# Kernel tuning notes

Measured on AMD Instinct MI355X. Metric: run time of the kernel, lower is better.

The kernel has to match this reference:

```python
import jax, jax.numpy as jnp
import numpy as np

D = 768
CTX = 64


def ln(x, g, b, eps=1e-5):
    m = x.mean(-1, keepdims=True)
    v = jnp.mean((x - m) ** 2, -1, keepdims=True)
    return (x - m) / jnp.sqrt(v + eps) * g + b


def setup_inputs() -> dict:
    key = jax.random.key(0)
    ks = jax.random.split(key, 16)
    B, N = 16, 1024
    w = lambda k, shape: jax.random.normal(k, shape, dtype=jnp.float32) * 0.02
    return {
        'comps': jax.random.normal(ks[0], (8, B, N, D), jnp.float32),
        'geometric_context': jax.random.normal(ks[1], (B, N, D), jnp.float32),
        'question_features': jax.random.normal(ks[2], (B, D), jnp.float32),
        'spatial_mask': jax.random.randint(ks[3], (B,), 0, 2) > 0,
        'gp_w1': w(ks[4], (D, D // 2)), 'gp_b1': jnp.zeros((D // 2,)),
        'gp_g1': jnp.ones((D // 2,)), 'gp_be1': jnp.zeros((D // 2,)),
        'gp_w2': w(ks[5], (D // 2, CTX)), 'gp_b2': jnp.zeros((CTX,)),
        'swp_w1': w(ks[6], (CTX + D, 256)), 'swp_b1': jnp.zeros((256,)),
        'swp_g1': jnp.ones((256,)), 'swp_be1': jnp.zeros((256,)),
        'swp_w2': w(ks[7], (256, 128)), 'swp_b2': jnp.zeros((128,)),
        'swp_g2': jnp.ones((128,)), 'swp_be2': jnp.zeros((128,)),
        'swp_w3': w(ks[8], (128, 8)), 'swp_b3': jnp.zeros((8,)),
        'sw1': w(ks[9], (4, D + CTX, D)), 'sb1': jnp.zeros((4, D)),
        'sg1': jnp.ones((4, D)), 'sbe1': jnp.zeros((4, D)),
        'sw2': w(ks[10], (4, D, D)), 'sb2': jnp.zeros((4, D)),
        'sg2': jnp.ones((4, D)), 'sbe2': jnp.zeros((4, D)),
        'rw1': w(ks[11], (4, D + CTX, D)), 'rb1': jnp.zeros((4, D)),
        'rg1': jnp.ones((4, D)), 'rbe1': jnp.zeros((4, D)),
        'rw2': w(ks[12], (4, D, D)), 'rb2': jnp.zeros((4, D)),
    }


def reference(comps, geometric_context, question_features, spatial_mask,
              gp_w1, gp_b1, gp_g1, gp_be1, gp_w2, gp_b2,
              swp_w1, swp_b1, swp_g1, swp_be1, swp_w2, swp_b2, swp_g2, swp_be2, swp_w3, swp_b3,
              sw1, sb1, sg1, sbe1, sw2, sb2, sg2, sbe2,
              rw1, rb1, rg1, rbe1, rw2, rb2):
    B, N = geometric_context.shape[:2]
    # geometric_processor on mean-pooled context -> [B, 64]
    gcc = jax.nn.relu(ln(geometric_context.mean(1) @ gp_w1 + gp_b1, gp_g1, gp_be1)) @ gp_w2 + gp_b2
    # spatial_weight_predictor -> softmax weights [B, 8]
    wi = jnp.concatenate([gcc, question_features], -1)
    h = jax.nn.gelu(ln(wi @ swp_w1 + swp_b1, swp_g1, swp_be1), approximate=False)
    h = jax.nn.gelu(ln(h @ swp_w2 + swp_b2, swp_g2, swp_be2), approximate=False)
    aw = jax.nn.softmax(h @ swp_w3 + swp_b3, -1)
    # expanded context; non-spatial samples use 0.1-scaled context for spatial-set comps
    ctx = jnp.broadcast_to(gcc[:, None, :], (B, N, CTX))
    ctx_s = ctx * jnp.where(spatial_mask, 1.0, 0.1)[:, None, None]
    # strong enhancers (GELU, second LN): P_unique(0), V_unique(1), PV(3), PT(5) - all spatial-set
    xs = jnp.concatenate([comps[jnp.array([0, 1, 3, 5])],
                          jnp.broadcast_to(ctx_s, (4, B, N, CTX))], -1)
    h = jax.nn.gelu(ln(jnp.einsum('kbnd,kdf->kbnf', xs, sw1) + sb1[:, None, None, :],
                       sg1[:, None, None, :], sbe1[:, None, None, :]), approximate=False)
    ys = ln(jnp.einsum('kbnd,kdf->kbnf', h, sw2) + sb2[:, None, None, :],
            sg2[:, None, None, :], sbe2[:, None, None, :])
    # ReLU enhancers (moderate/minimal share structure): TV(4, scaled ctx), T_unique(2), redundant(6), higher(7)
    ctx_r = jnp.stack([ctx_s, ctx, ctx, ctx], 0)
    xr = jnp.concatenate([comps[jnp.array([4, 2, 6, 7])], ctx_r], -1)
    h = jax.nn.relu(ln(jnp.einsum('kbnd,kdf->kbnf', xr, rw1) + rb1[:, None, None, :],
                       rg1[:, None, None, :], rbe1[:, None, None, :]))
    yr = jnp.einsum('kbnd,kdf->kbnf', h, rw2) + rb2[:, None, None, :]
    # non-spatial components pass through when spatial_mask is False
    m = spatial_mask[:, None, None]
    out = jnp.stack([
        ys[0],                              # P_unique
        ys[1],                              # V_unique
        jnp.where(m, yr[1], comps[2]),      # T_unique
        ys[2],                              # PV_synergy
        yr[0],                              # TV_synergy
        ys[3],                              # PT_synergy
        jnp.where(m, yr[2], comps[6]),      # redundant
        jnp.where(m, yr[3], comps[7]),      # higher_synergy
    ], 0)
    return out, aw
```

## Files before the change

kernel.cpp:

```cpp
#include <hip/hip_runtime.h>
#include <math.h>

#define MT 16384
#define DD 768
#define AW_OFF ((size_t)8 * MT * DD)

typedef __attribute__((ext_vector_type(8))) short short8;
typedef __attribute__((ext_vector_type(4))) float f32x4;
typedef __attribute__((ext_vector_type(4))) float fv4;
typedef __attribute__((ext_vector_type(4))) unsigned int u32x4;

#define OFF_W1T 0ULL
#define OFF_W2T 10223616ULL
#define OFF_Z1  19660800ULL
#define OFF_Z2  220987392ULL
#define OFF_GB  321650688ULL
#define OFF_P1  321675264ULL
#define OFF_P2  324820992ULL
#define OFF_ST1 326393856ULL
#define OFF_ST2 327442432ULL
#define OFF_GP  327966720ULL
#define OFF_GM  328359936ULL
#define OFF_CXS 328409088ULL
#define OFF_CXU 328411136ULL

static __device__ __forceinline__ unsigned short f2bf(float f) {
  unsigned u = __float_as_uint(f);
  u += 0x7fffu + ((u >> 16) & 1u);
  return (unsigned short)(u >> 16);
}
static __device__ __forceinline__ float bf2f(unsigned short h) {
  return __uint_as_float(((unsigned)h) << 16);
}
static __device__ __forceinline__ unsigned pk2(float lo, float hi) {
  return (unsigned)f2bf(lo) | ((unsigned)f2bf(hi) << 16);
}
static __device__ __forceinline__ float gelu_t(float y) {
  float y2 = y * y;
  float c = fmaf(y2, 0.0713548163f, 1.59576912161f);
  float e = __expf(-y * c);
  return y / (1.0f + e);
}
static __device__ __forceinline__ void gload_lds16(const void* g, void* l) {
  __builtin_amdgcn_global_load_lds(
      (const __attribute__((address_space(1))) void*)g,
      (__attribute__((address_space(3))) void*)l, 16, 0, 0);
}

__global__ void transpose_cvt(const float* sw1, const float* rw1,
                              const float* sw2, const float* rw2,
                              unsigned short* w1T, unsigned short* w2T) {
  __shared__ float t[32][33];
  const int z = blockIdx.z;
  int R; const float* sp; unsigned short* dp;
  if (z < 8) {
    R = 832;
    sp = ((z < 4) ? sw1 : rw1) + (size_t)(z & 3) * 832 * DD;
    dp = w1T + (size_t)z * DD * 832;
  } else {
    R = 768;
    int zz = z - 8;
    sp = ((zz < 4) ? sw2 : rw2) + (size_t)(zz & 3) * DD * DD;
    dp = w2T + (size_t)zz * DD * DD;
  }
  const int r0 = blockIdx.x * 32, c0 = blockIdx.y * 32;
  if (r0 >= R) return;
  const int tx = threadIdx.x & 31, ty = threadIdx.x >> 5;
#pragma unroll
  for (int i = 0; i < 4; i++) {
    int r = ty + i * 8;
    t[r][tx] = sp[(size_t)(r0 + r) * DD + c0 + tx];
  }
  __syncthreads();
#pragma unroll
  for (int i = 0; i < 4; i++) {
    int cc = ty + i * 8;
    dp[(size_t)(c0 + cc) * R + r0 + tx] = f2bf(t[tx][cc]);
  }
}

__global__ void pack_gb(const float* sg1, const float* sbe1,
                        const float* rg1, const float* rbe1,
                        unsigned short* gb1) {
  const int k = blockIdx.x * 256 + threadIdx.x;
  const int br = blockIdx.y;
  const float* gs = ((br < 4) ? sg1 : rg1) + (br & 3) * DD;
  const float* bs = ((br < 4) ? sbe1 : rbe1) + (br & 3) * DD;
  gb1[((size_t)br * DD + k) * 2]     = f2bf(gs[k]);
  gb1[((size_t)br * DD + k) * 2 + 1] = f2bf(bs[k]);
}

__global__ void colmean1(const float* __restrict__ geo, float* __restrict__ gp) {
  const int b = blockIdx.z, yc = blockIdx.y;
  const int col = blockIdx.x * 256 + threadIdx.x;
  const float* p = geo + (size_t)b * 1024 * DD + (size_t)yc * 128 * DD + col;
  float s = 0.f;
  for (int n = 0; n < 128; ++n) s += p[(size_t)n * DD];
  gp[((size_t)b * 8 + yc) * DD + col] = s;
}
__global__ void colmean2(const float* __restrict__ gp, float* __restrict__ gm) {
  const int b = blockIdx.y;
  const int col = blockIdx.x * 256 + threadIdx.x;
  float s = 0.f;
#pragma unroll
  for (int i = 0; i < 8; ++i) s += gp[((size_t)b * 8 + i) * DD + col];
  gm[(size_t)b * DD + col] = s * (1.0f / 1024.0f);
}

static __device__ float2 blk_sum2(float a, float b, float* red) {
  const int tid = threadIdx.x;
  __syncthreads();
  red[tid] = a; red[512 + tid] = b;
  if (tid < 128) { red[384 + tid] = 0.f; red[512 + 384 + tid] = 0.f; }
  __syncthreads();
  for (int s = 256; s > 0; s >>= 1) {
    if (tid < s) { red[tid] += red[tid + s]; red[512 + tid] += red[512 + tid + s]; }
    __syncthreads();
  }
  return make_float2(red[0], red[512]);
}

__global__ void small_mlp(
    const float* __restrict__ gc_mean, const float* __restrict__ qf,
    const int* __restrict__ mask,
    const float* __restrict__ gp_w1, const float* __restrict__ gp_b1,
    const float* __restrict__ gp_g1, const float* __restrict__ gp_be1,
    const float* __restrict__ gp_w2, const float* __restrict__ gp_b2,
    const float* __restrict__ swp_w1, const float* __restrict__ swp_b1,
    const float* __restrict__ swp_g1, const float* __restrict__ swp_be1,
    const float* __restrict__ swp_w2, const float* __restrict__ swp_b2,
    const float* __restrict__ swp_g2, const float* __restrict__ swp_be2,
    const float* __restrict__ swp_w3, const float* __restrict__ swp_b3,
    unsigned short* __restrict__ ctxs, unsigned short* __restrict__ ctxu,
    float* __restrict__ aw)
{
  __shared__ float gm[768];
  __shared__ float buf[832];
  __shared__ float tmp[384];
  __shared__ float red[1024];
  const int b = blockIdx.x, tid = threadIdx.x;

  for (int i = tid; i < 768; i += 384) gm[i] = gc_mean[b * 768 + i];
  __syncthreads();

  float z = gp_b1[tid];
  for (int k = 0; k < 768; k++) z += gm[k] * gp_w1[k * 384 + tid];
  float2 s = blk_sum2(z, z * z, red);
  {
    float mean = s.x * (1.f / 384.f);
    float rinv = rsqrtf(s.y * (1.f / 384.f) - mean * mean + 1e-5f);
    float y = (z - mean) * rinv * gp_g1[tid] + gp_be1[tid];
    tmp[tid] = fmaxf(y, 0.f);
  }
  __syncthreads();

  if (tid < 64) {
    float g = gp_b2[tid];
    for (int k = 0; k < 384; k++) g += tmp[k] * gp_w2[k * 64 + tid];
    float sc = (mask[b] != 0) ? 1.0f : 0.1f;
    ctxs[b * 64 + tid] = f2bf(g * sc);
    ctxu[b * 64 + tid] = f2bf(g);
    buf[tid] = g;
  }
  for (int i = tid; i < 768; i += 384) buf[64 + i] = qf[b * 768 + i];
  __syncthreads();

  float z1 = 0.f;
  if (tid < 256) {
    z1 = swp_b1[tid];
    for (int k = 0; k < 832; k++) z1 += buf[k] * swp_w1[k * 256 + tid];
  }
  s = blk_sum2(z1, z1 * z1, red);
  {
    float mean = s.x * (1.f / 256.f);
    float rinv = rsqrtf(s.y * (1.f / 256.f) - mean * mean + 1e-5f);
    if (tid < 256) {
      float y = (z1 - mean) * rinv * swp_g1[tid] + swp_be1[tid];
      tmp[tid] = 0.5f * y * (1.f + erff(y * 0.7071067811865476f));
    }
  }
  __syncthreads();

  float z2 = 0.f;
  if (tid < 128) {
    z2 = swp_b2[tid];
    for (int k = 0; k < 256; k++) z2 += tmp[k] * swp_w2[k * 128 + tid];
  }
  s = blk_sum2(z2, z2 * z2, red);
  {
    float mean = s.x * (1.f / 128.f);
    float rinv = rsqrtf(s.y * (1.f / 128.f) - mean * mean + 1e-5f);
    if (tid < 128) {
      float y = (z2 - mean) * rinv * swp_g2[tid] + swp_be2[tid];
      tmp[tid] = 0.5f * y * (1.f + erff(y * 0.7071067811865476f));
    }
  }
  __syncthreads();

  if (tid < 8) {
    float z3 = swp_b3[tid];
    for (int k = 0; k < 128; k++) z3 += tmp[k] * swp_w3[k * 8 + tid];
    buf[tid] = z3;
  }
  __syncthreads();
  if (tid < 8) {
    float mx = buf[0];
    for (int k = 1; k < 8; k++) mx = fmaxf(mx, buf[k]);
    float ssum = 0.f;
    for (int k = 0; k < 8; k++) ssum += expf(buf[k] - mx);
    aw[b * 8 + tid] = expf(buf[tid] - mx) / ssum;
  }
}

__global__ void stats_k(const float2* __restrict__ part, float2* __restrict__ st,
                        int nr) {
  int i = blockIdx.x * 256 + threadIdx.x;
  if (i >= nr) return;
  float2 p0 = part[i], p1 = part[nr + i], p2 = part[2 * nr + i];
  float s1 = p0.x + p1.x + p2.x, s2 = p0.y + p1.y + p2.y;
  float mean = s1 * (1.f / 768.f);
  float var = s2 * (1.f / 768.f) - mean * mean;
  float rinv = rsqrtf(var + 1e-5f);
  st[i] = make_float2(rinv, -mean * rinv);
}

__global__ __launch_bounds__(512, 2)
void gemm1_k(const float* __restrict__ comps,
             const unsigned short* __restrict__ cxs,
             const unsigned short* __restrict__ cxu,
             const unsigned short* __restrict__ w1T,
             const float* __restrict__ sb1, const float* __restrict__ rb1,
             unsigned short* __restrict__ z1,
             float2* __restrict__ part1,
             const int* __restrict__ mask)
{
  __shared__ __align__(16) unsigned short As[3][8192];
  __shared__ __align__(16) unsigned short Bs[3][8192];
  __shared__ float pscr[4][256][2];
  constexpr int NT = 26;

  const int id = blockIdx.x;
  const int x = id & 7, j = id >> 3;
  const int br_nt = j >> 3;
  const int mt = ((j & 7) << 3) | x;
  const int nt = br_nt % 3;
  const int br = br_nt / 3;
  const int m0 = mt * 256, n0 = nt * 256;
  const int b = m0 >> 10;
  const int msk = mask[b];
  if (br >= 5 && msk == 0) return;

  const int ci = (0x76245310u >> (br * 4)) & 15;
  const float* afp = comps + (size_t)ci * MT * DD + (size_t)m0 * DD;
  const unsigned short* ctxp = ((br <= 4) ? cxs : cxu) + b * 64;
  const unsigned short* wT = w1T + (size_t)br * DD * 832 + (size_t)n0 * 832;
  const float* bias = ((br < 4) ? sb1 : rb1) + (br & 3) * DD;
  unsigned short* zo = z1 + (size_t)br * MT * DD + (size_t)m0 * DD;

  const int tid = threadIdx.x;
  const int w = tid >> 6, lane = tid & 63, llo = lane & 15, lhi = lane >> 4;
  const int wm = w & 1, wn = w >> 1;
  const int q = tid & 3, rr = tid >> 2;
  const int swq = q ^ ((tid >> 3) & 3);

  const unsigned short* bsrc0 = wT + (size_t)rr * 832 + swq * 8;
  const unsigned short* bsrc1 = wT + (size_t)(128 + rr) * 832 + swq * 8;
  const float* asrc0 = afp + (size_t)rr * DD + q * 8;
  const float* asrc1 = afp + (size_t)(128 + rr) * DD + q * 8;
  const unsigned short* csrc = ctxp + q * 8;

  f32x4 acc[8][4];
#pragma unroll
  for (int mf = 0; mf < 8; ++mf)
#pragma unroll
    for (int nf = 0; nf < 4; ++nf) acc[mf][nf] = (f32x4)0.0f;

  struct St { fv4 f0, f1, f2, f3; u32x4 c; };

  auto issueB = [&](int kt, int s) {
    gload_lds16(bsrc0 + (size_t)kt * 32, &Bs[s][w * 512]);
    gload_lds16(bsrc1 + (size_t)kt * 32, &Bs[s][4096 + w * 512]);
  };
  auto issueA = [&](int kt) -> St {
    St s;
    if (kt < 24) {
      const float* p0 = asrc0 + kt * 32;
      s.f0 = *(const fv4*)p0; s.f1 = *(const fv4*)(p0 + 4);
      const float* p1 = asrc1 + kt * 32;
      s.f2 = *(const fv4*)p1; s.f3 = *(const fv4*)(p1 + 4);
    } else {
      s.c = *(const u32x4*)(csrc + (kt - 24) * 32);
    }
    return s;
  };
  auto commitA = [&](const St& s, int kt, int sl) {
    u32x4* d0 = (u32x4*)&As[sl][rr * 32 + swq * 8];
    u32x4* d1 = (u32x4*)&As[sl][(128 + rr) * 32 + swq * 8];
    if (kt < 24) {
      u32x4 v0, v1;
      v0[0] = pk2(s.f0[0], s.f0[1]); v0[1] = pk2(s.f0[2], s.f0[3]);
      v0[2] = pk2(s.f1[0], s.f1[1]); v0[3] = pk2(s.f1[2], s.f1[3]);
      v1[0] = pk2(s.f2[0], s.f2[1]); v1[1] = pk2(s.f2[2], s.f2[3]);
      v1[2] = pk2(s.f3[0], s.f3[1]); v1[3] = pk2(s.f3[2], s.f3[3]);
      *d0 = v0; *d1 = v1;
    } else {
      *d0 = s.c; *d1 = s.c;
    }
  };
  const int aswz = (lhi ^ ((llo >> 1) & 3)) << 3;
  const int arow0 = (wm * 128 + llo) * 32 + aswz;
  const int brow0 = (wn * 64 + llo) * 32 + aswz;
  auto compute = [&](int sl) {
    const unsigned short* Ab = &As[sl][0];
    const unsigned short* Bb = &Bs[sl][0];
    short8 bfr[4];
#pragma unroll
    for (int nf = 0; nf < 4; ++nf) bfr[nf] = *(const short8*)&Bb[brow0 + nf * 512];
#pragma unroll
    for (int mf = 0; mf < 8; ++mf) {
      short8 a = *(const short8*)&Ab[arow0 + mf * 512];
#pragma unroll
      for (int nf = 0; nf < 4; ++nf)
        acc[mf][nf] = __builtin_amdgcn_mfma_f32_16x16x32_bf16(a, bfr[nf], acc[mf][nf], 0, 0, 0);
    }
  };

  issueB(0, 0);
  __builtin_amdgcn_sched_barrier(0);
  St s0 = issueA(0);
  __builtin_amdgcn_sched_barrier(0);
  issueB(1, 1);
  __builtin_amdgcn_sched_barrier(0);
  St s1 = issueA(1);
  __builtin_amdgcn_sched_barrier(0);
  commitA(s0, 0, 0);
  asm volatile("s_waitcnt lgkmcnt(0)" ::: "memory");
  __builtin_amdgcn_sched_barrier(0);
  __builtin_amdgcn_s_barrier();

  St sCur = s1;
  int sl = 0;
#pragma unroll 1
  for (int t = 0; t < NT; ++t) {
    int sl1 = sl + 1; if (sl1 == 3) sl1 = 0;
    int sl2 = sl1 + 1; if (sl2 == 3) sl2 = 0;
    St sNxt = sCur;
    if (t + 2 < NT) {
      issueB(t + 2, sl2);
      __builtin_amdgcn_sched_barrier(0);
      sNxt = issueA(t + 2);
      __builtin_amdgcn_sched_barrier(0);
    }
    if (t + 1 < NT) commitA(sCur, t + 1, sl1);
    compute(sl);
    asm volatile("s_waitcnt lgkmcnt(0)" ::: "memory");
    __builtin_amdgcn_sched_barrier(0);
    __builtin_amdgcn_s_barrier();
    sCur = sNxt; sl = sl1;
  }

  const int n0w = n0 + wn * 64;
  float bia[4];
#pragma unroll
  for (int nf = 0; nf < 4; ++nf) bia[nf] = bias[n0w + nf * 16 + llo];
#pragma unroll
  for (int mf = 0; mf < 8; ++mf) {
#pragma unroll
    for (int r = 0; r < 4; ++r) {
      float zz[4]; float s1v = 0.f, s2v = 0.f;
#pragma unroll
      for (int nf = 0; nf < 4; ++nf) {
        float zv = acc[mf][nf][r] + bia[nf];
        zz[nf] = zv; s1v += zv; s2v += zv * zv;
      }
      const int rloc = wm * 128 + mf * 16 + lhi * 4 + r;
      const size_t rowoff = (size_t)rloc * DD;
#pragma unroll
      for (int nf = 0; nf < 4; ++nf) {
        float zon = __shfl_xor(zz[nf], 1);
        if ((llo & 1) == 0)
          *(unsigned*)&zo[rowoff + n0w + nf * 16 + llo] = pk2(zz[nf], zon);
      }
#pragma unroll
      for (int d = 1; d < 16; d <<= 1) {
        s1v += __shfl_xor(s1v, d); s2v += __shfl_xor(s2v, d);
      }
      if (llo == 0) { pscr[wn][rloc][0] = s1v; pscr[wn][rloc][1] = s2v; }
    }
  }
  __syncthreads();
  if (tid < 256) {
    float a = 0.f, c = 0.f;
#pragma unroll
    for (int qq = 0; qq < 4; ++qq) { a += pscr[qq][tid][0]; c += pscr[qq][tid][1]; }
    part1[(size_t)nt * (8 * MT) + (size_t)br * MT + m0 + tid] = make_float2(a, c);
  }
}

template<int SBR>
__global__ __launch_bounds__(512, 2)
void gemm2_k(const float* __restrict__ comps,
             const unsigned short* __restrict__ z1,
             const float2* __restrict__ st1,
             const unsigned short* __restrict__ gb1,
             const unsigned short* __restrict__ w2T,
             const float* __restrict__ sb2, const float* __restrict__ rb2,
             unsigned short* __restrict__ z2,
             float2* __restrict__ part2,
             float* __restrict__ outp,
             const int* __restrict__ mask)
{
  __shared__ __align__(16) unsigned short As[3][8192];
  __shared__ __align__(16) unsigned short Bs[3][8192];
  __shared__ float pscr[4][256][2];
  constexpr int NT = 24;

  const int id = blockIdx.x;
  const int x = id & 7, j = id >> 3;
  const int br_nt = j >> 3;
  const int mt = ((j & 7) << 3) | x;
  const int nt = br_nt % 3;
  const int brl = br_nt / 3;
  const int br = SBR ? brl : (brl + 4);
  const int m0 = mt * 256, n0 = nt * 256;
  const int b = m0 >> 10;
  const int msk = mask[b];
  const int ci = (0x76245310u >> (br * 4)) & 15;
  const int tid = threadIdx.x;

  if (!SBR && br >= 5 && msk == 0) {
    const float* cs = comps + (size_t)ci * MT * DD + (size_t)m0 * DD + n0;
    float* cd = outp + (size_t)ci * MT * DD + (size_t)m0 * DD + n0;
#pragma unroll 1
    for (int k = 0; k < 32; ++k) {
      int idx = tid + k * 512;
      int r2 = idx >> 6, c4 = (idx & 63) * 4;
      *(fv4*)(cd + (size_t)r2 * DD + c4) = *(const fv4*)(cs + (size_t)r2 * DD + c4);
    }
    return;
  }

  const unsigned short* az = z1 + (size_t)br * MT * DD + (size_t)m0 * DD;
  const unsigned short* wT = w2T + (size_t)br * DD * DD + (size_t)n0 * DD;
  const float* bias = (SBR ? sb2 : rb2) + (br & 3) * DD;

  const int w = tid >> 6, lane = tid & 63, llo = lane & 15, lhi = lane >> 4;
  const int wm = w & 1, wn = w >> 1;
  const int q = tid & 3, rr = tid >> 2;
  const int swq = q ^ ((tid >> 3) & 3);

  const unsigned short* bsrc0 = wT + (size_t)rr * DD + swq * 8;
  const unsigned short* bsrc1 = wT + (size_t)(128 + rr) * DD + swq * 8;
  const unsigned short* zsrc0 = az + (size_t)rr * DD + q * 8;
  const unsigned short* zsrc1 = az + (size_t)(128 + rr) * DD + q * 8;
  const unsigned short* gsrc = gb1 + (size_t)br * DD * 2 + q * 16;
  const float2 stv0 = st1[(size_t)br * MT + m0 + rr];
  const float2 stv1 = st1[(size_t)br * MT + m0 + 128 + rr];

  f32x4 acc[8][4];
#pragma unroll
  for (int mf = 0; mf < 8; ++mf)
#pragma unroll
    for (int nf = 0; nf < 4; ++nf) acc[mf][nf] = (f32x4)0.0f;

  struct St { u32x4 z0, z1v, g0, g1; };

  auto issueB = [&](int kt, int s) {
    gload_lds16(bsrc0 + (size_t)kt * 32, &Bs[s][w * 512]);
    gload_lds16(bsrc1 + (size_t)kt * 32, &Bs[s][4096 + w * 512]);
  };
  auto issueA = [&](int kt) -> St {
    St s;
    s.z0  = *(const u32x4*)(zsrc0 + kt * 32);
    s.z1v = *(const u32x4*)(zsrc1 + kt * 32);
    s.g0  = *(const u32x4*)(gsrc + kt * 64);
    s.g1  = *(const u32x4*)(gsrc + kt * 64 + 8);
    return s;
  };
  auto xform2 = [&](unsigned zw, unsigned gwa, unsigned gwb, float2 stv) -> unsigned {
    float z0 = bf2f((unsigned short)(zw & 0xffffu));
    float z1f = bf2f((unsigned short)(zw >> 16));
    float g0 = bf2f((unsigned short)(gwa & 0xffffu));
    float be0 = bf2f((unsigned short)(gwa >> 16));
    float g1 = bf2f((unsigned short)(gwb & 0xffffu));
    float be1 = bf2f((unsigned short)(gwb >> 16));
    float y0 = fmaf(fmaf(z0, stv.x, stv.y), g0, be0);
    float y1 = fmaf(fmaf(z1f, stv.x, stv.y), g1, be1);
    if (SBR) { y0 = gelu_t(y0); y1 = gelu_t(y1); }
    else     { y0 = fmaxf(y0, 0.f); y1 = fmaxf(y1, 0.f); }
    return pk2(y0, y1);
  };
  auto commitA2 = [&](const St& s, int sl) {
    u32x4 v0, v1;
    v0[0] = xform2(s.z0[0], s.g0[0], s.g0[1], stv0);
    v0[1] = xform2(s.z0[1], s.g0[2], s.g0[3], stv0);
    v0[2] = xform2(s.z0[2], s.g1[0], s.g1[1], stv0);
    v0[3] = xform2(s.z0[3], s.g1[2], s.g1[3], stv0);
    v1[0] = xform2(s.z1v[0], s.g0[0], s.g0[1], stv1);
    v1[1] = xform2(s.z1v[1], s.g0[2], s.g0[3], stv1);
    v1[2] = xform2(s.z1v[2], s.g1[0], s.g1[1], stv1);
    v1[3] = xform2(s.z1v[3], s.g1[2], s.g1[3], stv1);
    *(u32x4*)&As[sl][rr * 32 + swq * 8] = v0;
    *(u32x4*)&As[sl][(128 + rr) * 32 + swq * 8] = v1;
  };

  const int aswz = (lhi ^ ((llo >> 1) & 3)) << 3;
  const int arow0 = (wm * 128 + llo) * 32 + aswz;
  const int brow0 = (wn * 64 + llo) * 32 + aswz;
  auto compute = [&](int sl) {
    const unsigned short* Ab = &As[sl][0];
    const unsigned short* Bb = &Bs[sl][0];
    short8 bfr[4];
#pragma unroll
    for (int nf = 0; nf < 4; ++nf) bfr[nf] = *(const short8*)&Bb[brow0 + nf * 512];
#pragma unroll
    for (int mf = 0; mf < 8; ++mf) {
      short8 a = *(const short8*)&Ab[arow0 + mf * 512];
#pragma unroll
      for (int nf = 0; nf < 4; ++nf)
        acc[mf][nf] = __builtin_amdgcn_mfma_f32_16x16x32_bf16(a, bfr[nf], acc[mf][nf], 0, 0, 0);
    }
  };

  issueB(0, 0);
  __builtin_amdgcn_sched_barrier(0);
  St s0 = issueA(0);
  __builtin_amdgcn_sched_barrier(0);
  issueB(1, 1);
  __builtin_amdgcn_sched_barrier(0);
  St s1 = issueA(1);
  __builtin_amdgcn_sched_barrier(0);
  commitA2(s0, 0);
  asm volatile("s_waitcnt lgkmcnt(0)" ::: "memory");
  __builtin_amdgcn_sched_barrier(0);
  __builtin_amdgcn_s_barrier();

  St sCur = s1;
  int sl = 0;
#pragma unroll 1
  for (int t = 0; t < NT; ++t) {
    int sl1 = sl + 1; if (sl1 == 3) sl1 = 0;
    int sl2 = sl1 + 1; if (sl2 == 3) sl2 = 0;
    St sNxt = sCur;
    if (t + 2 < NT) {
      issueB(t + 2, sl2);
      __builtin_amdgcn_sched_barrier(0);
      sNxt = issueA(t + 2);
      __builtin_amdgcn_sched_barrier(0);
    }
    if (t + 1 < NT) commitA2(sCur, sl1);
    compute(sl);
    asm volatile("s_waitcnt lgkmcnt(0)" ::: "memory");
    __builtin_amdgcn_sched_barrier(0);
    __builtin_amdgcn_s_barrier();
    sCur = sNxt; sl = sl1;
  }

  const int n0w = n0 + wn * 64;
  float bia[4];
#pragma unroll
  for (int nf = 0; nf < 4; ++nf) bia[nf] = bias[n0w + nf * 16 + llo];

  if (SBR) {
    unsigned short* zo = z2 + (size_t)br * MT * DD + (size_t)m0 * DD;
#pragma unroll
    for (int mf = 0; mf < 8; ++mf) {
#pragma unroll
      for (int r = 0; r < 4; ++r) {
        float zz[4]; float s1v = 0.f, s2v = 0.f;
#pragma unroll
        for (int nf = 0; nf < 4; ++nf) {
          float zv = acc[mf][nf][r] + bia[nf];
          zz[nf] = zv; s1v += zv; s2v += zv * zv;
        }
        const int rloc = wm * 128 + mf * 16 + lhi * 4 + r;
        const size_t rowoff = (size_t)rloc * DD;
#pragma unroll
        for (int nf = 0; nf < 4; ++nf) {
          float zon = __shfl_xor(zz[nf], 1);
          if ((llo & 1) == 0)
            *(unsigned*)&zo[rowoff + n0w + nf * 16 + llo] = pk2(zz[nf], zon);
        }
#pragma unroll
        for (int d = 1; d < 16; d <<= 1) {
          s1v += __shfl_xor(s1v, d); s2v += __shfl_xor(s2v, d);
        }
        if (llo == 0) { pscr[wn][rloc][0] = s1v; pscr[wn][rloc][1] = s2v; }
      }
    }
    __syncthreads();
    if (tid < 256) {
      float a = 0.f, c = 0.f;
#pragma unroll
      for (int qq = 0; qq < 4; ++qq) { a += pscr[qq][tid][0]; c += pscr[qq][tid][1]; }
      part2[(size_t)nt * (4 * MT) + (size_t)br * MT + m0 + tid] = make_float2(a, c);
    }
  } else {
    float* fo = outp + (size_t)ci * MT * DD + (size_t)m0 * DD;
#pragma unroll
    for (int mf = 0; mf < 8; ++mf) {
#pragma unroll
      for (int r = 0; r < 4; ++r) {
        const int rloc = wm * 128 + mf * 16 + lhi * 4 + r;
        const size_t rowoff = (size_t)rloc * DD;
#pragma unroll
        for (int nf = 0; nf < 4; ++nf)
          fo[rowoff + n0w + nf * 16 + llo] = acc[mf][nf][r] + bia[nf];
      }
    }
  }
}

__global__ void finish_s(const unsigned short* __restrict__ z2,
                         const float2* __restrict__ st2,
                         const float* __restrict__ sg2,
                         const float* __restrict__ sbe2,
                         float* __restrict__ outp)
{
  const int tid = threadIdx.x;
  const int rowg = blockIdx.x * 8 + (tid >> 5);
  const int l = tid & 31;
  const int br = rowg >> 14;
  const int r = rowg & 16383;
  const int ci = (0x5310u >> (br * 4)) & 15;
  const unsigned short* zp = z2 + (size_t)rowg * DD;
  float* op = outp + (size_t)ci * MT * DD + (size_t)r * DD;
  const float2 stv = st2[rowg];
  const float* g = sg2 + br * DD;
  const float* be = sbe2 + br * DD;
#pragma unroll
  for (int c = 0; c < 3; ++c) {
    const int col = l * 8 + c * 256;
    u32x4 zv = *(const u32x4*)(zp + col);
    fv4 ga = *(const fv4*)(g + col), gb = *(const fv4*)(g + col + 4);
    fv4 ba = *(const fv4*)(be + col), bb = *(const fv4*)(be + col + 4);
    fv4 o0, o1;
#pragma unroll
    for (int wd = 0; wd < 2; ++wd) {
      o0[2 * wd]     = fmaf(fmaf(bf2f((unsigned short)(zv[wd] & 0xffffu)), stv.x, stv.y), ga[2 * wd], ba[2 * wd]);
      o0[2 * wd + 1] = fmaf(fmaf(bf2f((unsigned short)(zv[wd] >> 16)), stv.x, stv.y), ga[2 * wd + 1], ba[2 * wd + 1]);
      o1[2 * wd]     = fmaf(fmaf(bf2f((unsigned short)(zv[wd + 2] & 0xffffu)), stv.x, stv.y), gb[2 * wd], bb[2 * wd]);
      o1[2 * wd + 1] = fmaf(fmaf(bf2f((unsigned short)(zv[wd + 2] >> 16)), stv.x, stv.y), gb[2 * wd + 1], bb[2 * wd + 1]);
    }
    *(fv4*)(op + col) = o0;
    *(fv4*)(op + col + 4) = o1;
  }
}

extern "C" void kernel_launch(void* const* d_in, const int* in_sizes, int n_in,
                              void* d_out, int out_size, void* d_ws, size_t ws_size,
                              hipStream_t stream)
{
  (void)in_sizes; (void)n_in; (void)out_size; (void)ws_size;
  const float* comps  = (const float*)d_in[0];
  const float* geo    = (const float*)d_in[1];
  const float* qf     = (const float*)d_in[2];
  const int*   mask   = (const int*)d_in[3];
  const float* gp_w1  = (const float*)d_in[4];
  const float* gp_b1  = (const float*)d_in[5];
  const float* gp_g1  = (const float*)d_in[6];
  const float* gp_be1 = (const float*)d_in[7];
  const float* gp_w2  = (const float*)d_in[8];
  const float* gp_b2  = (const float*)d_in[9];
  const float* swp_w1 = (const float*)d_in[10];
  const float* swp_b1 = (const float*)d_in[11];
  const float* swp_g1 = (const float*)d_in[12];
  const float* swp_be1= (const float*)d_in[13];
  const float* swp_w2 = (const float*)d_in[14];
  const float* swp_b2 = (const float*)d_in[15];
  const float* swp_g2 = (const float*)d_in[16];
  const float* swp_be2= (const float*)d_in[17];
  const float* swp_w3 = (const float*)d_in[18];
  const float* swp_b3 = (const float*)d_in[19];
  const float* sw1 = (const float*)d_in[20];
  const float* sb1 = (const float*)d_in[21];
  const float* sg1 = (const float*)d_in[22];
  const float* sbe1= (const float*)d_in[23];
  const float* sw2 = (const float*)d_in[24];
  const float* sb2 = (const float*)d_in[25];
  const float* sg2 = (const float*)d_in[26];
  const float* sbe2= (const float*)d_in[27];
  const float* rw1 = (const float*)d_in[28];
  const float* rb1 = (const float*)d_in[29];
  const float* rg1 = (const float*)d_in[30];
  const float* rbe1= (const float*)d_in[31];
  const float* rw2 = (const float*)d_in[32];
  const float* rb2 = (const float*)d_in[33];
  float* out = (float*)d_out;

  char* ws = (char*)d_ws;
  unsigned short* w1T = (unsigned short*)(ws + OFF_W1T);
  unsigned short* w2T = (unsigned short*)(ws + OFF_W2T);
  unsigned short* z1  = (unsigned short*)(ws + OFF_Z1);
  unsigned short* z2  = (unsigned short*)(ws + OFF_Z2);
  unsigned short* gb1 = (unsigned short*)(ws + OFF_GB);
  float2* part1 = (float2*)(ws + OFF_P1);
  float2* part2 = (float2*)(ws + OFF_P2);
  float2* st1   = (float2*)(ws + OFF_ST1);
  float2* st2   = (float2*)(ws + OFF_ST2);
  float* gpart  = (float*)(ws + OFF_GP);
  float* gmean  = (float*)(ws + OFF_GM);
  unsigned short* cxs = (unsigned short*)(ws + OFF_CXS);
  unsigned short* cxu = (unsigned short*)(ws + OFF_CXU);

  transpose_cvt<<<dim3(26, 24, 16), 256, 0, stream>>>(sw1, rw1, sw2, rw2, w1T, w2T);
  pack_gb<<<dim3(3, 8), 256, 0, stream>>>(sg1, sbe1, rg1, rbe1, gb1);
  colmean1<<<dim3(3, 8, 16), 256, 0, stream>>>(geo, gpart);
  colmean2<<<dim3(3, 16), 256, 0, stream>>>(gpart, gmean);
  small_mlp<<<16, 384, 0, stream>>>(gmean, qf, mask,
      gp_w1, gp_b1, gp_g1, gp_be1, gp_w2, gp_b2,
      swp_w1, swp_b1, swp_g1, swp_be1, swp_w2, swp_b2, swp_g2, swp_be2,
      swp_w3, swp_b3, cxs, cxu, out + AW_OFF);

  hipMemsetAsync(part1, 0, 3 * 8 * MT * sizeof(float2), stream);
  hipMemsetAsync(part2, 0, 3 * 4 * MT * sizeof(float2), stream);

  gemm1_k<<<1536, 512, 0, stream>>>(comps, cxs, cxu, w1T, sb1, rb1, z1, part1, mask);
  stats_k<<<512, 256, 0, stream>>>(part1, st1, 8 * MT);
  gemm2_k<1><<<768, 512, 0, stream>>>(comps, z1, st1, gb1, w2T, sb2, rb2,
                                      z2, part2, out, mask);
  gemm2_k<0><<<768, 512, 0, stream>>>(comps, z1, st1, gb1, w2T, sb2, rb2,
                                      z2, part2, out, mask);
  stats_k<<<256, 256, 0, stream>>>(part2, st2, 4 * MT);
  finish_s<<<8192, 256, 0, stream>>>(z2, st2, sg2, sbe2, out);
}
```

Baseline: 950.6 us.

## Split LN1+activation into separate kernel, shrink GEMM M-tile, direct-to-LDS A loads

Moves the first LayerNorm normalization and GELU/ReLU out of the second GEMM's A-load path into a standalone act1_k kernel that writes a bf16 activation buffer. With that buffer, gemm2 can stream A straight into LDS like B does, using a 3-stage pipeline. Both GEMMs switch to 128-row M tiles with a 4-block occupancy hint, gemm1 drops to double buffering, and the two templated gemm2 launches merge into one. The cost is an extra full read and write of the z1-sized activation tensor plus an extra launch. The part1/part2 memsets are removed, which relies on every partial-sum slot being overwritten each call.

After: 774.7 us. 1.23x faster.

```diff
diff --git a/kernel.cpp b/kernel.cpp
--- a/kernel.cpp
+++ b/kernel.cpp
@@ -14,7 +14,6 @@
 #define OFF_W2T 10223616ULL
 #define OFF_Z1  19660800ULL
 #define OFF_Z2  220987392ULL
-#define OFF_GB  321650688ULL
 #define OFF_P1  321675264ULL
 #define OFF_P2  324820992ULL
 #define OFF_ST1 326393856ULL
@@ -23,6 +22,7 @@
 #define OFF_GM  328359936ULL
 #define OFF_CXS 328409088ULL
 #define OFF_CXU 328411136ULL
+#define OFF_A1  335544320ULL
 
 static __device__ __forceinline__ unsigned short f2bf(float f) {
   unsigned u = __float_as_uint(f);
@@ -77,17 +77,6 @@
     int cc = ty + i * 8;
     dp[(size_t)(c0 + cc) * R + r0 + tx] = f2bf(t[tx][cc]);
   }
-}
-
-__global__ void pack_gb(const float* sg1, const float* sbe1,
-                        const float* rg1, const float* rbe1,
-                        unsigned short* gb1) {
-  const int k = blockIdx.x * 256 + threadIdx.x;
-  const int br = blockIdx.y;
-  const float* gs = ((br < 4) ? sg1 : rg1) + (br & 3) * DD;
-  const float* bs = ((br < 4) ? sbe1 : rbe1) + (br & 3) * DD;
-  gb1[((size_t)br * DD + k) * 2]     = f2bf(gs[k]);
-  gb1[((size_t)br * DD + k) * 2 + 1] = f2bf(bs[k]);
 }
 
 __global__ void colmean1(const float* __restrict__ geo, float* __restrict__ gp) {
@@ -224,7 +213,7 @@
   st[i] = make_float2(rinv, -mean * rinv);
 }
 
-__global__ __launch_bounds__(512, 2)
+__global__ __launch_bounds__(512, 4)
 void gemm1_k(const float* __restrict__ comps,
              const unsigned short* __restrict__ cxs,
              const unsigned short* __restrict__ cxu,
@@ -234,137 +223,128 @@
              float2* __restrict__ part1,
              const int* __restrict__ mask)
 {
-  __shared__ __align__(16) unsigned short As[3][8192];
-  __shared__ __align__(16) unsigned short Bs[3][8192];
-  __shared__ float pscr[4][256][2];
+  __shared__ __align__(16) unsigned short As[2][4096];
+  __shared__ __align__(16) unsigned short Bs[2][8192];
+  __shared__ float pscr[4][128][2];
   constexpr int NT = 26;
 
   const int id = blockIdx.x;
   const int x = id & 7, j = id >> 3;
-  const int br_nt = j >> 3;
-  const int mt = ((j & 7) << 3) | x;
+  const int br_nt = j >> 4;
+  const int mt = ((j & 15) << 3) | x;
   const int nt = br_nt % 3;
   const int br = br_nt / 3;
-  const int m0 = mt * 256, n0 = nt * 256;
+  const int m0 = mt * 128, n0 = nt * 256;
   const int b = m0 >> 10;
-  const int msk = mask[b];
-  if (br >= 5 && msk == 0) return;
+  if (br >= 5 && mask[b] == 0) return;
 
   const int ci = (0x76245310u >> (br * 4)) & 15;
   const float* afp = comps + (size_t)ci * MT * DD + (size_t)m0 * DD;
   const unsigned short* ctxp = ((br <= 4) ? cxs : cxu) + b * 64;
   const unsigned short* wT = w1T + (size_t)br * DD * 832 + (size_t)n0 * 832;
-  const float* bias = ((br < 4) ? sb1 : rb1) + (br & 3) * DD;
-  unsigned short* zo = z1 + (size_t)br * MT * DD + (size_t)m0 * DD;
 
   const int tid = threadIdx.x;
   const int w = tid >> 6, lane = tid & 63, llo = lane & 15, lhi = lane >> 4;
   const int wm = w & 1, wn = w >> 1;
-  const int q = tid & 3, rr = tid >> 2;
-  const int swq = q ^ ((tid >> 3) & 3);
-
-  const unsigned short* bsrc0 = wT + (size_t)rr * 832 + swq * 8;
-  const unsigned short* bsrc1 = wT + (size_t)(128 + rr) * 832 + swq * 8;
-  const float* asrc0 = afp + (size_t)rr * DD + q * 8;
-  const float* asrc1 = afp + (size_t)(128 + rr) * DD + q * 8;
-  const unsigned short* csrc = ctxp + q * 8;
-
-  f32x4 acc[8][4];
-#pragma unroll
-  for (int mf = 0; mf < 8; ++mf)
+
+  const int arow = tid >> 2, ap = tid & 3;
+  const int aslot = (arow * 32 + ((ap ^ ((arow >> 1) & 3)) << 3));
+  const float* asrc = afp + (size_t)arow * DD + ap * 8;
+  const unsigned short* csrc = ctxp + ap * 8;
+
+  const int q = lane & 3, rrB = w * 16 + (lane >> 2);
+  const int swqB = q ^ ((rrB >> 1) & 3);
+  const unsigned short* bsrc0 = wT + (size_t)rrB * 832 + swqB * 8;
+  const unsigned short* bsrc1 = wT + (size_t)(128 + rrB) * 832 + swqB * 8;
+
+  f32x4 acc[4][4];
+#pragma unroll
+  for (int mf = 0; mf < 4; ++mf)
 #pragma unroll
     for (int nf = 0; nf < 4; ++nf) acc[mf][nf] = (f32x4)0.0f;
 
-  struct St { fv4 f0, f1, f2, f3; u32x4 c; };
+  struct St { u32x4 q0, q1; };
 
   auto issueB = [&](int kt, int s) {
     gload_lds16(bsrc0 + (size_t)kt * 32, &Bs[s][w * 512]);
     gload_lds16(bsrc1 + (size_t)kt * 32, &Bs[s][4096 + w * 512]);
   };
-  auto issueA = [&](int kt) -> St {
+  auto loadA = [&](int kt) -> St {
     St s;
     if (kt < 24) {
-      const float* p0 = asrc0 + kt * 32;
-      s.f0 = *(const fv4*)p0; s.f1 = *(const fv4*)(p0 + 4);
-      const float* p1 = asrc1 + kt * 32;
-      s.f2 = *(const fv4*)p1; s.f3 = *(const fv4*)(p1 + 4);
+      const u32x4* p = (const u32x4*)(asrc + kt * 32);
+      s.q0 = p[0]; s.q1 = p[1];
     } else {
-      s.c = *(const u32x4*)(csrc + (kt - 24) * 32);
+      s.q0 = *(const u32x4*)(csrc + (kt - 24) * 32);
+      s.q1 = s.q0;
     }
     return s;
   };
   auto commitA = [&](const St& s, int kt, int sl) {
-    u32x4* d0 = (u32x4*)&As[sl][rr * 32 + swq * 8];
-    u32x4* d1 = (u32x4*)&As[sl][(128 + rr) * 32 + swq * 8];
+    u32x4 v;
     if (kt < 24) {
-      u32x4 v0, v1;
-      v0[0] = pk2(s.f0[0], s.f0[1]); v0[1] = pk2(s.f0[2], s.f0[3]);
-      v0[2] = pk2(s.f1[0], s.f1[1]); v0[3] = pk2(s.f1[2], s.f1[3]);
-      v1[0] = pk2(s.f2[0], s.f2[1]); v1[1] = pk2(s.f2[2], s.f2[3]);
-      v1[2] = pk2(s.f3[0], s.f3[1]); v1[3] = pk2(s.f3[2], s.f3[3]);
-      *d0 = v0; *d1 = v1;
+      v[0] = pk2(__uint_as_float(s.q0[0]), __uint_as_float(s.q0[1]));
+      v[1] = pk2(__uint_as_float(s.q0[2]), __uint_as_float(s.q0[3]));
+      v[2] = pk2(__uint_as_float(s.q1[0]), __uint_as_float(s.q1[1]));
+      v[3] = pk2(__uint_as_float(s.q1[2]), __uint_as_float(s.q1[3]));
     } else {
-      *d0 = s.c; *d1 = s.c;
-    }
+      v = s.q0;
+    }
+    *(u32x4*)&As[sl][aslot] = v;
   };
+
   const int aswz = (lhi ^ ((llo >> 1) & 3)) << 3;
-  const int arow0 = (wm * 128 + llo) * 32 + aswz;
+  const int arow0 = (wm * 64 + llo) * 32 + aswz;
   const int brow0 = (wn * 64 + llo) * 32 + aswz;
   auto compute = [&](int sl) {
-    const unsigned short* Ab = &As[sl][0];
-    const unsigned short* Bb = &Bs[sl][0];
-    short8 bfr[4];
-#pragma unroll
-    for (int nf = 0; nf < 4; ++nf) bfr[nf] = *(const short8*)&Bb[brow0 + nf * 512];
-#pragma unroll
-    for (int mf = 0; mf < 8; ++mf) {
-      short8 a = *(const short8*)&Ab[arow0 + mf * 512];
-#pragma unroll
-      for (int nf = 0; nf < 4; ++nf)
-        acc[mf][nf] = __builtin_amdgcn_mfma_f32_16x16x32_bf16(a, bfr[nf], acc[mf][nf], 0, 0, 0);
+    short8 afr[4];
+#pragma unroll
+    for (int mf = 0; mf < 4; ++mf)
+      afr[mf] = *(const short8*)&As[sl][arow0 + mf * 512];
+#pragma unroll
+    for (int nf = 0; nf < 4; ++nf) {
+      short8 bfr = *(const short8*)&Bs[sl][brow0 + nf * 512];
+#pragma unroll
+      for (int mf = 0; mf < 4; ++mf)
+        acc[mf][nf] = __builtin_amdgcn_mfma_f32_16x16x32_bf16(afr[mf], bfr, acc[mf][nf], 0, 0, 0);
     }
   };
 
   issueB(0, 0);
-  __builtin_amdgcn_sched_barrier(0);
-  St s0 = issueA(0);
-  __builtin_amdgcn_sched_barrier(0);
-  issueB(1, 1);
-  __builtin_amdgcn_sched_barrier(0);
-  St s1 = issueA(1);
-  __builtin_amdgcn_sched_barrier(0);
-  commitA(s0, 0, 0);
+  {
+    St s0 = loadA(0);
+    commitA(s0, 0, 0);
+  }
   asm volatile("s_waitcnt lgkmcnt(0)" ::: "memory");
   __builtin_amdgcn_sched_barrier(0);
   __builtin_amdgcn_s_barrier();
 
-  St sCur = s1;
-  int sl = 0;
 #pragma unroll 1
   for (int t = 0; t < NT; ++t) {
-    int sl1 = sl + 1; if (sl1 == 3) sl1 = 0;
-    int sl2 = sl1 + 1; if (sl2 == 3) sl2 = 0;
-    St sNxt = sCur;
-    if (t + 2 < NT) {
-      issueB(t + 2, sl2);
-      __builtin_amdgcn_sched_barrier(0);
-      sNxt = issueA(t + 2);
-      __builtin_amdgcn_sched_barrier(0);
-    }
-    if (t + 1 < NT) commitA(sCur, t + 1, sl1);
-    compute(sl);
+    const int cur = t & 1, nxt = cur ^ 1;
+    const bool more = (t + 1 < NT);
+    St sn;
+    if (more) {
+      issueB(t + 1, nxt);
+      sn = loadA(t + 1);
+    }
+    __builtin_amdgcn_sched_barrier(0);
+    compute(cur);
+    __builtin_amdgcn_sched_barrier(0);
+    if (more) commitA(sn, t + 1, nxt);
     asm volatile("s_waitcnt lgkmcnt(0)" ::: "memory");
     __builtin_amdgcn_sched_barrier(0);
     __builtin_amdgcn_s_barrier();
-    sCur = sNxt; sl = sl1;
-  }
-
+  }
+
+  const float* bias = ((br < 4) ? sb1 : rb1) + (br & 3) * DD;
+  unsigned short* zo = z1 + (size_t)br * MT * DD + (size_t)m0 * DD;
   const int n0w = n0 + wn * 64;
   float bia[4];
 #pragma unroll
   for (int nf = 0; nf < 4; ++nf) bia[nf] = bias[n0w + nf * 16 + llo];
 #pragma unroll
-  for (int mf = 0; mf < 8; ++mf) {
+  for (int mf = 0; mf < 4; ++mf) {
 #pragma unroll
     for (int r = 0; r < 4; ++r) {
       float zz[4]; float s1v = 0.f, s2v = 0.f;
@@ -373,7 +353,7 @@
         float zv = acc[mf][nf][r] + bia[nf];
         zz[nf] = zv; s1v += zv; s2v += zv * zv;
       }
-      const int rloc = wm * 128 + mf * 16 + lhi * 4 + r;
+      const int rloc = wm * 64 + mf * 16 + lhi * 4 + r;
       const size_t rowoff = (size_t)rloc * DD;
 #pragma unroll
       for (int nf = 0; nf < 4; ++nf) {
@@ -389,7 +369,7 @@
     }
   }
   __syncthreads();
-  if (tid < 256) {
+  if (tid < 128) {
     float a = 0.f, c = 0.f;
 #pragma unroll
     for (int qq = 0; qq < 4; ++qq) { a += pscr[qq][tid][0]; c += pscr[qq][tid][1]; }
@@ -397,12 +377,55 @@
   }
 }
 
-template<int SBR>
-__global__ __launch_bounds__(512, 2)
+__global__ void act1_k(const unsigned short* __restrict__ z1,
+                       const float2* __restrict__ st1,
+                       const float* __restrict__ sg1, const float* __restrict__ sbe1,
+                       const float* __restrict__ rg1, const float* __restrict__ rbe1,
+                       const int* __restrict__ mask,
+                       unsigned short* __restrict__ a1)
+{
+  const int tid = threadIdx.x;
+  const int rowg = blockIdx.x * 8 + (tid >> 5);
+  const int l = tid & 31;
+  const int br = rowg >> 14;
+  const int r = rowg & 16383;
+  const int b = r >> 10;
+  if (br >= 5 && mask[b] == 0) return;
+  const bool isg = (br < 4);
+  const float* g  = (isg ? sg1  + br * DD : rg1  + (br - 4) * DD);
+  const float* be = (isg ? sbe1 + br * DD : rbe1 + (br - 4) * DD);
+  const float2 stv = st1[rowg];
+  const unsigned short* zp = z1 + (size_t)rowg * DD;
+  unsigned short* op = a1 + (size_t)rowg * DD;
+#pragma unroll
+  for (int c = 0; c < 3; ++c) {
+    const int col = l * 8 + c * 256;
+    u32x4 zv = *(const u32x4*)(zp + col);
+    fv4 ga = *(const fv4*)(g + col), gb = *(const fv4*)(g + col + 4);
+    fv4 ba = *(const fv4*)(be + col), bb = *(const fv4*)(be + col + 4);
+    float y[8];
+#pragma unroll
+    for (int wd = 0; wd < 2; ++wd) {
+      y[2*wd]   = fmaf(fmaf(bf2f((unsigned short)(zv[wd] & 0xffffu)), stv.x, stv.y), ga[2*wd], ba[2*wd]);
+      y[2*wd+1] = fmaf(fmaf(bf2f((unsigned short)(zv[wd] >> 16)), stv.x, stv.y), ga[2*wd+1], ba[2*wd+1]);
+      y[4+2*wd]   = fmaf(fmaf(bf2f((unsigned short)(zv[wd+2] & 0xffffu)), stv.x, stv.y), gb[2*wd], bb[2*wd]);
+      y[4+2*wd+1] = fmaf(fmaf(bf2f((unsigned short)(zv[wd+2] >> 16)), stv.x, stv.y), gb[2*wd+1], bb[2*wd+1]);
+    }
+    u32x4 ov;
+#pragma unroll
+    for (int wd = 0; wd < 4; ++wd) {
+      float y0 = y[2*wd], y1 = y[2*wd+1];
+      if (isg) { y0 = gelu_t(y0); y1 = gelu_t(y1); }
+      else     { y0 = fmaxf(y0, 0.f); y1 = fmaxf(y1, 0.f); }
+      ov[wd] = pk2(y0, y1);
+    }
+    *(u32x4*)(op + col) = ov;
+  }
+}
+
+__global__ __launch_bounds__(512, 4)
 void gemm2_k(const float* __restrict__ comps,
-             const unsigned short* __restrict__ z1,
-             const float2* __restrict__ st1,
-             const unsigned short* __restrict__ gb1,
+             const unsigned short* __restrict__ a1,
              const unsigned short* __restrict__ w2T,
              const float* __restrict__ sb2, const float* __restrict__ rb2,
              unsigned short* __restrict__ z2,
@@ -410,29 +433,27 @@
              float* __restrict__ outp,
              const int* __restrict__ mask)
 {
-  __shared__ __align__(16) unsigned short As[3][8192];
+  __shared__ __align__(16) unsigned short As[3][4096];
   __shared__ __align__(16) unsigned short Bs[3][8192];
-  __shared__ float pscr[4][256][2];
+  __shared__ float pscr[4][128][2];
   constexpr int NT = 24;
 
   const int id = blockIdx.x;
   const int x = id & 7, j = id >> 3;
-  const int br_nt = j >> 3;
-  const int mt = ((j & 7) << 3) | x;
+  const int br_nt = j >> 4;
+  const int mt = ((j & 15) << 3) | x;
   const int nt = br_nt % 3;
-  const int brl = br_nt / 3;
-  const int br = SBR ? brl : (brl + 4);
-  const int m0 = mt * 256, n0 = nt * 256;
+  const int br = br_nt / 3;
+  const int m0 = mt * 128, n0 = nt * 256;
   const int b = m0 >> 10;
-  const int msk = mask[b];
   const int ci = (0x76245310u >> (br * 4)) & 15;
   const int tid = threadIdx.x;
 
-  if (!SBR && br >= 5 && msk == 0) {
+  if (br >= 5 && mask[b] == 0) {
     const float* cs = comps + (size_t)ci * MT * DD + (size_t)m0 * DD + n0;
     float* cd = outp + (size_t)ci * MT * DD + (size_t)m0 * DD + n0;
 #pragma unroll 1
-    for (int k = 0; k < 32; ++k) {
+    for (int k = 0; k < 16; ++k) {
       int idx = tid + k * 512;
       int r2 = idx >> 6, c4 = (idx & 63) * 4;
       *(fv4*)(cd + (size_t)r2 * DD + c4) = *(const fv4*)(cs + (size_t)r2 * DD + c4);
@@ -440,131 +461,79 @@
     return;
   }
 
-  const unsigned short* az = z1 + (size_t)br * MT * DD + (size_t)m0 * DD;
+  const unsigned short* az = a1 + (size_t)br * MT * DD + (size_t)m0 * DD;
   const unsigned short* wT = w2T + (size_t)br * DD * DD + (size_t)n0 * DD;
-  const float* bias = (SBR ? sb2 : rb2) + (br & 3) * DD;
 
   const int w = tid >> 6, lane = tid & 63, llo = lane & 15, lhi = lane >> 4;
   const int wm = w & 1, wn = w >> 1;
-  const int q = tid & 3, rr = tid >> 2;
-  const int swq = q ^ ((tid >> 3) & 3);
-
-  const unsigned short* bsrc0 = wT + (size_t)rr * DD + swq * 8;
-  const unsigned short* bsrc1 = wT + (size_t)(128 + rr) * DD + swq * 8;
-  const unsigned short* zsrc0 = az + (size_t)rr * DD + q * 8;
-  const unsigned short* zsrc1 = az + (size_t)(128 + rr) * DD + q * 8;
-  const unsigned short* gsrc = gb1 + (size_t)br * DD * 2 + q * 16;
-  const float2 stv0 = st1[(size_t)br * MT + m0 + rr];
-  const float2 stv1 = st1[(size_t)br * MT + m0 + 128 + rr];
-
-  f32x4 acc[8][4];
-#pragma unroll
-  for (int mf = 0; mf < 8; ++mf)
+  const int q = lane & 3, rrB = w * 16 + (lane >> 2);
+  const int swqB = q ^ ((rrB >> 1) & 3);
+
+  const unsigned short* asrcD = az + (size_t)rrB * DD + swqB * 8;
+  const unsigned short* bsrc0 = wT + (size_t)rrB * DD + swqB * 8;
+  const unsigned short* bsrc1 = wT + (size_t)(128 + rrB) * DD + swqB * 8;
+
+  f32x4 acc[4][4];
+#pragma unroll
+  for (int mf = 0; mf < 4; ++mf)
 #pragma unroll
     for (int nf = 0; nf < 4; ++nf) acc[mf][nf] = (f32x4)0.0f;
 
-  struct St { u32x4 z0, z1v, g0, g1; };
-
-  auto issueB = [&](int kt, int s) {
+  auto issueT = [&](int kt, int s) {
+    gload_lds16(asrcD + (size_t)kt * 32, &As[s][w * 512]);
     gload_lds16(bsrc0 + (size_t)kt * 32, &Bs[s][w * 512]);
     gload_lds16(bsrc1 + (size_t)kt * 32, &Bs[s][4096 + w * 512]);
   };
-  auto issueA = [&](int kt) -> St {
-    St s;
-    s.z0  = *(const u32x4*)(zsrc0 + kt * 32);
-    s.z1v = *(const u32x4*)(zsrc1 + kt * 32);
-    s.g0  = *(const u32x4*)(gsrc + kt * 64);
-    s.g1  = *(const u32x4*)(gsrc + kt * 64 + 8);
-    return s;
-  };
-  auto xform2 = [&](unsigned zw, unsigned gwa, unsigned gwb, float2 stv) -> unsigned {
-    float z0 = bf2f((unsigned short)(zw & 0xffffu));
-    float z1f = bf2f((unsigned short)(zw >> 16));
-    float g0 = bf2f((unsigned short)(gwa & 0xffffu));
-    float be0 = bf2f((unsigned short)(gwa >> 16));
-    float g1 = bf2f((unsigned short)(gwb & 0xffffu));
-    float be1 = bf2f((unsigned short)(gwb >> 16));
-    float y0 = fmaf(fmaf(z0, stv.x, stv.y), g0, be0);
-    float y1 = fmaf(fmaf(z1f, stv.x, stv.y), g1, be1);
-    if (SBR) { y0 = gelu_t(y0); y1 = gelu_t(y1); }
-    else     { y0 = fmaxf(y0, 0.f); y1 = fmaxf(y1, 0.f); }
-    return pk2(y0, y1);
-  };
-  auto commitA2 = [&](const St& s, int sl) {
-    u32x4 v0, v1;
-    v0[0] = xform2(s.z0[0], s.g0[0], s.g0[1], stv0);
-    v0[1] = xform2(s.z0[1], s.g0[2], s.g0[3], stv0);
-    v0[2] = xform2(s.z0[2], s.g1[0], s.g1[1], stv0);
-    v0[3] = xform2(s.z0[3], s.g1[2], s.g1[3], stv0);
-    v1[0] = xform2(s.z1v[0], s.g0[0], s.g0[1], stv1);
-    v1[1] = xform2(s.z1v[1], s.g0[2], s.g0[3], stv1);
-    v1[2] = xform2(s.z1v[2], s.g1[0], s.g1[1], stv1);
-    v1[3] = xform2(s.z1v[3], s.g1[2], s.g1[3], stv1);
-    *(u32x4*)&As[sl][rr * 32 + swq * 8] = v0;
-    *(u32x4*)&As[sl][(128 + rr) * 32 + swq * 8] = v1;
-  };
 
   const int aswz = (lhi ^ ((llo >> 1) & 3)) << 3;
-  const int arow0 = (wm * 128 + llo) * 32 + aswz;
+  const int arow0 = (wm * 64 + llo) * 32 + aswz;
   const int brow0 = (wn * 64 + llo) * 32 + aswz;
   auto compute = [&](int sl) {
-    const unsigned short* Ab = &As[sl][0];
-    const unsigned short* Bb = &Bs[sl][0];
-    short8 bfr[4];
-#pragma unroll
-    for (int nf = 0; nf < 4; ++nf) bfr[nf] = *(const short8*)&Bb[brow0 + nf * 512];
-#pragma unroll
-    for (int mf = 0; mf < 8; ++mf) {
-      short8 a = *(const short8*)&Ab[arow0 + mf * 512];
-#pragma unroll
-      for (int nf = 0; nf < 4; ++nf)
-        acc[mf][nf] = __builtin_amdgcn_mfma_f32_16x16x32_bf16(a, bfr[nf], acc[mf][nf], 0, 0, 0);
+    short8 afr[4];
+#pragma unroll
+    for (int mf = 0; mf < 4; ++mf)
+      afr[mf] = *(const short8*)&As[sl][arow0 + mf * 512];
+#pragma unroll
+    for (int nf = 0; nf < 4; ++nf) {
+      short8 bfr = *(const short8*)&Bs[sl][brow0 + nf * 512];
+#pragma unroll
+      for (int mf = 0; mf < 4; ++mf)
+        acc[mf][nf] = __builtin_amdgcn_mfma_f32_16x16x32_bf16(afr[mf], bfr, acc[mf][nf], 0, 0, 0);
     }
   };
 
-  issueB(0, 0);
-  __builtin_amdgcn_sched_barrier(0);
-  St s0 = issueA(0);
-  __builtin_amdgcn_sched_barrier(0);
-  issueB(1, 1);
-  __builtin_amdgcn_sched_barrier(0);
-  St s1 = issueA(1);
-  __builtin_amdgcn_sched_barrier(0);
-  commitA2(s0, 0);
-  asm volatile("s_waitcnt lgkmcnt(0)" ::: "memory");
+  issueT(0, 0);
+  issueT(1, 1);
+  asm volatile("s_waitcnt vmcnt(3)" ::: "memory");
   __builtin_amdgcn_sched_barrier(0);
   __builtin_amdgcn_s_barrier();
 
-  St sCur = s1;
   int sl = 0;
 #pragma unroll 1
   for (int t = 0; t < NT; ++t) {
-    int sl1 = sl + 1; if (sl1 == 3) sl1 = 0;
-    int sl2 = sl1 + 1; if (sl2 == 3) sl2 = 0;
-    St sNxt = sCur;
-    if (t + 2 < NT) {
-      issueB(t + 2, sl2);
-      __builtin_amdgcn_sched_barrier(0);
-      sNxt = issueA(t + 2);
-      __builtin_amdgcn_sched_barrier(0);
-    }
-    if (t + 1 < NT) commitA2(sCur, sl1);
+    int sl2 = sl + 2; if (sl2 >= 3) sl2 -= 3;
+    const bool more = (t + 2 < NT);
+    if (more) issueT(t + 2, sl2);
+    __builtin_amdgcn_sched_barrier(0);
     compute(sl);
+    if (more) asm volatile("s_waitcnt vmcnt(3)" ::: "memory");
+    else      asm volatile("s_waitcnt vmcnt(0)" ::: "memory");
     asm volatile("s_waitcnt lgkmcnt(0)" ::: "memory");
     __builtin_amdgcn_sched_barrier(0);
     __builtin_amdgcn_s_barrier();
-    sCur = sNxt; sl = sl1;
+    ++sl; if (sl == 3) sl = 0;
   }
 
   const int n0w = n0 + wn * 64;
+  const float* bias = ((br < 4) ? sb2 : rb2) + (br & 3) * DD;
   float bia[4];
 #pragma unroll
   for (int nf = 0; nf < 4; ++nf) bia[nf] = bias[n0w + nf * 16 + llo];
 
-  if (SBR) {
+  if (br < 4) {
     unsigned short* zo = z2 + (size_t)br * MT * DD + (size_t)m0 * DD;
 #pragma unroll
-    for (int mf = 0; mf < 8; ++mf) {
+    for (int mf = 0; mf < 4; ++mf) {
 #pragma unroll
       for (int r = 0; r < 4; ++r) {
         float zz[4]; float s1v = 0.f, s2v = 0.f;
@@ -573,7 +542,7 @@
           float zv = acc[mf][nf][r] + bia[nf];
           zz[nf] = zv; s1v += zv; s2v += zv * zv;
         }
-        const int rloc = wm * 128 + mf * 16 + lhi * 4 + r;
+        const int rloc = wm * 64 + mf * 16 + lhi * 4 + r;
         const size_t rowoff = (size_t)rloc * DD;
 #pragma unroll
         for (int nf = 0; nf < 4; ++nf) {
@@ -589,7 +558,7 @@
       }
     }
     __syncthreads();
-    if (tid < 256) {
+    if (tid < 128) {
       float a = 0.f, c = 0.f;
 #pragma unroll
       for (int qq = 0; qq < 4; ++qq) { a += pscr[qq][tid][0]; c += pscr[qq][tid][1]; }
@@ -598,10 +567,10 @@
   } else {
     float* fo = outp + (size_t)ci * MT * DD + (size_t)m0 * DD;
 #pragma unroll
-    for (int mf = 0; mf < 8; ++mf) {
+    for (int mf = 0; mf < 4; ++mf) {
 #pragma unroll
       for (int r = 0; r < 4; ++r) {
-        const int rloc = wm * 128 + mf * 16 + lhi * 4 + r;
+        const int rloc = wm * 64 + mf * 16 + lhi * 4 + r;
         const size_t rowoff = (size_t)rloc * DD;
 #pragma unroll
         for (int nf = 0; nf < 4; ++nf)
@@ -693,7 +662,6 @@
   unsigned short* w2T = (unsigned short*)(ws + OFF_W2T);
   unsigned short* z1  = (unsigned short*)(ws + OFF_Z1);
   unsigned short* z2  = (unsigned short*)(ws + OFF_Z2);
-  unsigned short* gb1 = (unsigned short*)(ws + OFF_GB);
   float2* part1 = (float2*)(ws + OFF_P1);
   float2* part2 = (float2*)(ws + OFF_P2);
   float2* st1   = (float2*)(ws + OFF_ST1);
@@ -702,9 +670,9 @@
   float* gmean  = (float*)(ws + OFF_GM);
   unsigned short* cxs = (unsigned short*)(ws + OFF_CXS);
   unsigned short* cxu = (unsigned short*)(ws + OFF_CXU);
+  unsigned short* a1  = (unsigned short*)(ws + OFF_A1);
 
   transpose_cvt<<<dim3(26, 24, 16), 256, 0, stream>>>(sw1, rw1, sw2, rw2, w1T, w2T);
-  pack_gb<<<dim3(3, 8), 256, 0, stream>>>(sg1, sbe1, rg1, rbe1, gb1);
   colmean1<<<dim3(3, 8, 16), 256, 0, stream>>>(geo, gpart);
   colmean2<<<dim3(3, 16), 256, 0, stream>>>(gpart, gmean);
   small_mlp<<<16, 384, 0, stream>>>(gmean, qf, mask,
@@ -712,15 +680,10 @@
       swp_w1, swp_b1, swp_g1, swp_be1, swp_w2, swp_b2, swp_g2, swp_be2,
       swp_w3, swp_b3, cxs, cxu, out + AW_OFF);
 
-  hipMemsetAsync(part1, 0, 3 * 8 * MT * sizeof(float2), stream);
-  hipMemsetAsync(part2, 0, 3 * 4 * MT * sizeof(float2), stream);
-
-  gemm1_k<<<1536, 512, 0, stream>>>(comps, cxs, cxu, w1T, sb1, rb1, z1, part1, mask);
+  gemm1_k<<<3072, 512, 0, stream>>>(comps, cxs, cxu, w1T, sb1, rb1, z1, part1, mask);
   stats_k<<<512, 256, 0, stream>>>(part1, st1, 8 * MT);
-  gemm2_k<1><<<768, 512, 0, stream>>>(comps, z1, st1, gb1, w2T, sb2, rb2,
-                                      z2, part2, out, mask);
-  gemm2_k<0><<<768, 512, 0, stream>>>(comps, z1, st1, gb1, w2T, sb2, rb2,
-                                      z2, part2, out, mask);
+  act1_k<<<16384, 256, 0, stream>>>(z1, st1, sg1, sbe1, rg1, rbe1, mask, a1);
+  gemm2_k<<<3072, 512, 0, stream>>>(comps, a1, w2T, sb2, rb2, z2, part2, out, mask);
   stats_k<<<256, 256, 0, stream>>>(part2, st2, 4 * MT);
   finish_s<<<8192, 256, 0, stream>>>(z2, st2, sg2, sbe2, out);
 }
```
